# Kernel tuning notes

Hardware: AMD Instinct MI355X
Metric: run time of the kernel (lower is better)

Reference implementation:

```python
import jax, jax.numpy as jnp
import numpy as np

N = 1024
B = 128

def setup_inputs() -> dict:
    key = jax.random.key(0)
    k1, k2 = jax.random.split(key)
    log_alpha = jax.random.normal(k1, (B, N), dtype=jnp.float32)
    W = jax.random.normal(k2, (N, N), dtype=jnp.float32)  # unnormalized_transition_matrix
    return {"log_alpha": log_alpha, "W": W}

def reference(log_alpha, W):
    # log_softmax over dim=0 (columns) as in torch F.log_softmax(..., dim=0)
    log_T = jax.nn.log_softmax(W, axis=0)  # (N, N)
    # out[b, i] = logsumexp_k( log_T[i, k] + log_alpha[b, k] )
    # matches log_domain_matmul(log_T, log_alpha.T).T
    scores = log_T[None, :, :] + log_alpha[:, None, :]  # (B, N, N)
    out = jax.scipy.special.logsumexp(scores, axis=2)   # (B, N)
    return out
```

## Files before the change

### kernel.cpp

```cpp
#include <hip/hip_runtime.h>
#include <hip/hip_bf16.h>

#define N 1024
#define B 128

typedef __attribute__((ext_vector_type(8))) short short8;
typedef __attribute__((ext_vector_type(4))) float float4v;


__global__ void expw_colsum_kernel(const float* __restrict__ W,
                                   __hip_bfloat16* __restrict__ expW,
                                   float* __restrict__ pS) {
    int k  = blockIdx.x * 256 + threadIdx.x;
    int r0 = blockIdx.y * 16;
    float s = 0.f;
    #pragma unroll
    for (int r = r0; r < r0 + 16; ++r) {
        float e = __expf(W[r * N + k]);
        s += e;
        expW[r * N + k] = __float2bfloat16(e);
    }
    pS[blockIdx.y * N + k] = s;
}

__global__ void expa_kernel(const float* __restrict__ LA,
                            const float* __restrict__ pS,
                            __hip_bfloat16* __restrict__ expA) {
    int k = blockIdx.x * 256 + threadIdx.x;
    float S = 0.f;
    #pragma unroll
    for (int y = 0; y < 64; ++y) S += pS[y * N + k];
    float inv = __frcp_rn(S);
    int b0 = blockIdx.y * 4;
    #pragma unroll
    for (int b = b0; b < b0 + 4; ++b)
        expA[b * N + k] = __float2bfloat16(__expf(LA[b * N + k]) * inv);
}

__global__ void lse_gemm_kernel(const __hip_bfloat16* __restrict__ expA,
                                const __hip_bfloat16* __restrict__ expW,
                                float* __restrict__ out) {
    int lane = threadIdx.x & 63;
    int wave = threadIdx.x >> 6;
    int i0 = (blockIdx.x >> 1) * 16;
    int b0 = ((blockIdx.x & 1) * 4 + wave) * 16;
    int row  = lane & 15;
    int quad = lane >> 4;

    const short* aP = (const short*)(expA + (b0 + row) * N + quad * 8);
    const short* bP = (const short*)(expW + (i0 + row) * N + quad * 8);

    float4v acc = {0.f, 0.f, 0.f, 0.f};
    #pragma unroll 8
    for (int kk = 0; kk < N; kk += 32) {
        short8 af = *(const short8*)(aP + kk);
        short8 bf = *(const short8*)(bP + kk);
        acc = __builtin_amdgcn_mfma_f32_16x16x32_bf16(af, bf, acc, 0, 0, 0);
    }

    #pragma unroll
    for (int r = 0; r < 4; ++r) {
        int bb = b0 + quad * 4 + r;
        out[bb * N + i0 + row] = __logf(acc[r]);
    }
}

extern "C" void kernel_launch(void* const* d_in, const int* in_sizes, int n_in,
                              void* d_out, int out_size, void* d_ws, size_t ws_size,
                              hipStream_t stream) {
    const float* LA = (const float*)d_in[0];
    const float* W  = (const float*)d_in[1];
    float* out = (float*)d_out;

    char* ws = (char*)d_ws;
    float* pS = (float*)(ws);
    __hip_bfloat16* expW = (__hip_bfloat16*)(ws + 262144);
    __hip_bfloat16* expA = (__hip_bfloat16*)(ws + 262144 + 2097152);

    expw_colsum_kernel<<<dim3(4, 64), 256, 0, stream>>>(W, expW, pS);
    expa_kernel<<<dim3(4, 32), 256, 0, stream>>>(LA, pS, expA);
    lse_gemm_kernel<<<128, 256, 0, stream>>>(expA, expW, out);
}
```

Baseline: 83.86 us.

## Fuse three kernels into one persistent kernel with software grid barriers

Merges the exp/column-sum, alpha-normalization and bf16 MFMA GEMM kernels into a single 256-block launch separated by atomic sense-reversal grid barriers. The aim is to remove the cost of two extra kernel launches and the gaps between them. It depends on all 256 blocks being co-resident to avoid deadlock, and adds spin-wait and fence overhead while only 128 blocks do work in the GEMM phase.

```diff
diff --git a/kernel.cpp b/kernel.cpp
--- a/kernel.cpp
+++ b/kernel.cpp
@@ -8,60 +8,88 @@
 typedef __attribute__((ext_vector_type(4))) float float4v;
 
 
-__global__ void expw_colsum_kernel(const float* __restrict__ W,
-                                   __hip_bfloat16* __restrict__ expW,
-                                   float* __restrict__ pS) {
-    int k  = blockIdx.x * 256 + threadIdx.x;
-    int r0 = blockIdx.y * 16;
-    float s = 0.f;
-    #pragma unroll
-    for (int r = r0; r < r0 + 16; ++r) {
-        float e = __expf(W[r * N + k]);
-        s += e;
-        expW[r * N + k] = __float2bfloat16(e);
+__device__ __attribute__((aligned(128))) int g_arrive = 0;
+__device__ __attribute__((aligned(128))) int g_sense  = 0;
+
+__device__ __forceinline__ void grid_barrier() {
+    __syncthreads();
+    if (threadIdx.x == 0) {
+        __threadfence();
+        int epoch = __hip_atomic_load(&g_sense, __ATOMIC_RELAXED, __HIP_MEMORY_SCOPE_AGENT);
+        int prev  = __hip_atomic_fetch_add(&g_arrive, 1, __ATOMIC_ACQ_REL, __HIP_MEMORY_SCOPE_AGENT);
+        if (prev == (int)gridDim.x - 1) {
+            __hip_atomic_store(&g_arrive, 0, __ATOMIC_RELAXED, __HIP_MEMORY_SCOPE_AGENT);
+            __hip_atomic_store(&g_sense, epoch + 1, __ATOMIC_RELEASE, __HIP_MEMORY_SCOPE_AGENT);
+        } else {
+            while (__hip_atomic_load(&g_sense, __ATOMIC_ACQUIRE, __HIP_MEMORY_SCOPE_AGENT) == epoch)
+                __builtin_amdgcn_s_sleep(1);
+        }
+        __threadfence();
     }
-    pS[blockIdx.y * N + k] = s;
+    __syncthreads();
 }
 
-__global__ void expa_kernel(const float* __restrict__ LA,
-                            const float* __restrict__ pS,
-                            __hip_bfloat16* __restrict__ expA) {
-    int k = blockIdx.x * 256 + threadIdx.x;
-    float S = 0.f;
-    #pragma unroll
-    for (int y = 0; y < 64; ++y) S += pS[y * N + k];
-    float inv = __frcp_rn(S);
-    int b0 = blockIdx.y * 4;
-    #pragma unroll
-    for (int b = b0; b < b0 + 4; ++b)
-        expA[b * N + k] = __float2bfloat16(__expf(LA[b * N + k]) * inv);
-}
+__global__ void __launch_bounds__(256) fused_kernel(
+    const float* __restrict__ LA, const float* __restrict__ W,
+    float* __restrict__ out, float* __restrict__ pS,
+    __hip_bfloat16* __restrict__ expW, __hip_bfloat16* __restrict__ expA)
+{
+    const int tid = threadIdx.x;
+    const int blk = blockIdx.x;
 
-__global__ void lse_gemm_kernel(const __hip_bfloat16* __restrict__ expA,
-                                const __hip_bfloat16* __restrict__ expW,
-                                float* __restrict__ out) {
-    int lane = threadIdx.x & 63;
-    int wave = threadIdx.x >> 6;
-    int i0 = (blockIdx.x >> 1) * 16;
-    int b0 = ((blockIdx.x & 1) * 4 + wave) * 16;
-    int row  = lane & 15;
-    int quad = lane >> 4;
-
-    const short* aP = (const short*)(expA + (b0 + row) * N + quad * 8);
-    const short* bP = (const short*)(expW + (i0 + row) * N + quad * 8);
-
-    float4v acc = {0.f, 0.f, 0.f, 0.f};
-    #pragma unroll 8
-    for (int kk = 0; kk < N; kk += 32) {
-        short8 af = *(const short8*)(aP + kk);
-        short8 bf = *(const short8*)(bP + kk);
-        acc = __builtin_amdgcn_mfma_f32_16x16x32_bf16(af, bf, acc, 0, 0, 0);
+    {
+        int k  = (blk & 3) * 256 + tid;
+        int r0 = (blk >> 2) * 16;
+        float s = 0.f;
+        #pragma unroll
+        for (int r = r0; r < r0 + 16; ++r) {
+            float e = __expf(W[r * N + k]);
+            s += e;
+            expW[r * N + k] = __float2bfloat16(e);
+        }
+        pS[(blk >> 2) * N + k] = s;
     }
 
-    #pragma unroll
-    for (int r = 0; r < 4; ++r) {
-        int bb = b0 + quad * 4 + r;
-        out[bb * N + i0 + row] = __logf(acc[r]);
+    grid_barrier();
+
+    {
+        int k = (blk & 3) * 256 + tid;
+        float S = 0.f;
+        #pragma unroll
+        for (int y = 0; y < 64; ++y) S += pS[y * N + k];
+        float inv = __frcp_rn(S);
+        int b0 = (blk >> 2) * 2;
+        #pragma unroll
+        for (int b = b0; b < b0 + 2; ++b)
+            expA[b * N + k] = __float2bfloat16(__expf(LA[b * N + k]) * inv);
+    }
+
+    grid_barrier();
+
+    if (blk < 128) {
+        int lane = tid & 63;
+        int wave = tid >> 6;
+        int i0 = (blk >> 1) * 16;
+        int b0 = ((blk & 1) * 4 + wave) * 16;
+        int row  = lane & 15;
+        int quad = lane >> 4;
+
+        const short* aP = (const short*)(expA + (b0 + row) * N + quad * 8);
+        const short* bP = (const short*)(expW + (i0 + row) * N + quad * 8);
+
+        float4v acc = {0.f, 0.f, 0.f, 0.f};
+        #pragma unroll 8
+        for (int kk = 0; kk < N; kk += 32) {
+            short8 af = *(const short8*)(aP + kk);
+            short8 bf = *(const short8*)(bP + kk);
+            acc = __builtin_amdgcn_mfma_f32_16x16x32_bf16(af, bf, acc, 0, 0, 0);
+        }
+
+        #pragma unroll
+        for (int r = 0; r < 4; ++r) {
+            int bb = b0 + quad * 4 + r;
+            out[bb * N + i0 + row] = __logf(acc[r]);
+        }
     }
 }
 
@@ -77,7 +105,5 @@
     __hip_bfloat16* expW = (__hip_bfloat16*)(ws + 262144);
     __hip_bfloat16* expA = (__hip_bfloat16*)(ws + 262144 + 2097152);
 
-    expw_colsum_kernel<<<dim3(4, 64), 256, 0, stream>>>(W, expW, pS);
-    expa_kernel<<<dim3(4, 32), 256, 0, stream>>>(LA, pS, expA);
-    lse_gemm_kernel<<<128, 256, 0, stream>>>(expA, expW, out);
+    fused_kernel<<<256, 256, 0, stream>>>(LA, W, out, pS, expW, expA);
 }
```

Result: slower. 123.8 us (+47.6%).

## Fuse exp of W and log_alpha into GEMM kernel, drop intermediate bf16 buffers

Applied to the files above, without the earlier changes.

Removes the expA kernel and the bf16 expW write. The GEMM kernel now computes exp(W) for its 16 rows directly into XOR-swizzled shared memory, and the column-sum reciprocals into shared memory. It also computes exp(log_alpha)*invS on the fly for the A operand. This cuts one launch and the global round-trips of the intermediates, at the cost of redundant exp work: each W row tile is exponentiated by two blocks, and each block recomputes all 1024 inverse sums from 64 partials.

```diff
diff --git a/kernel.cpp b/kernel.cpp
--- a/kernel.cpp
+++ b/kernel.cpp
@@ -8,53 +8,78 @@
 typedef __attribute__((ext_vector_type(4))) float float4v;
 
 
-__global__ void expw_colsum_kernel(const float* __restrict__ W,
-                                   __hip_bfloat16* __restrict__ expW,
-                                   float* __restrict__ pS) {
+static __device__ __forceinline__ short bf16bits(float x) {
+    union { __hip_bfloat16 h; short s; } u;
+    u.h = __float2bfloat16(x);
+    return u.s;
+}
+
+__global__ void __launch_bounds__(256) colsum_kernel(const float* __restrict__ W,
+                                                     float* __restrict__ pS) {
     int k  = blockIdx.x * 256 + threadIdx.x;
     int r0 = blockIdx.y * 16;
     float s = 0.f;
     #pragma unroll
-    for (int r = r0; r < r0 + 16; ++r) {
-        float e = __expf(W[r * N + k]);
-        s += e;
-        expW[r * N + k] = __float2bfloat16(e);
-    }
+    for (int r = r0; r < r0 + 16; ++r)
+        s += __expf(W[r * N + k]);
     pS[blockIdx.y * N + k] = s;
 }
 
-__global__ void expa_kernel(const float* __restrict__ LA,
-                            const float* __restrict__ pS,
-                            __hip_bfloat16* __restrict__ expA) {
-    int k = blockIdx.x * 256 + threadIdx.x;
-    float S = 0.f;
+__global__ void __launch_bounds__(256) lse_kernel(const float* __restrict__ LA,
+                                                  const float* __restrict__ W,
+                                                  const float* __restrict__ pS,
+                                                  float* __restrict__ out) {
+    __shared__ float invS[N];
+    __shared__ short bt[16 * N];
+
+    const int tid = threadIdx.x;
+    const int i0  = (blockIdx.x >> 1) * 16;
+
     #pragma unroll
-    for (int y = 0; y < 64; ++y) S += pS[y * N + k];
-    float inv = __frcp_rn(S);
-    int b0 = blockIdx.y * 4;
-    #pragma unroll
-    for (int b = b0; b < b0 + 4; ++b)
-        expA[b * N + k] = __float2bfloat16(__expf(LA[b * N + k]) * inv);
-}
+    for (int r = 0; r < 16; ++r) {
+        #pragma unroll
+        for (int j = 0; j < 4; ++j) {
+            int c = j * 256 + tid;
+            float e = __expf(W[(i0 + r) * N + c]);
+            int byte = ((r * N + c) * 2) ^ ((r & 7) << 4);
+            *(short*)((char*)bt + byte) = bf16bits(e);
+        }
+    }
 
-__global__ void lse_gemm_kernel(const __hip_bfloat16* __restrict__ expA,
-                                const __hip_bfloat16* __restrict__ expW,
-                                float* __restrict__ out) {
-    int lane = threadIdx.x & 63;
-    int wave = threadIdx.x >> 6;
-    int i0 = (blockIdx.x >> 1) * 16;
-    int b0 = ((blockIdx.x & 1) * 4 + wave) * 16;
+    for (int k = tid; k < N; k += 256) {
+        float s = 0.f;
+        #pragma unroll
+        for (int y = 0; y < 64; ++y) s += pS[y * N + k];
+        invS[k] = __frcp_rn(s);
+    }
+    __syncthreads();
+
+    int lane = tid & 63;
+    int wave = tid >> 6;
+    int b0   = (blockIdx.x & 1) * 64 + wave * 16;
     int row  = lane & 15;
     int quad = lane >> 4;
+    const int xm = (row & 7) << 4;
 
-    const short* aP = (const short*)(expA + (b0 + row) * N + quad * 8);
-    const short* bP = (const short*)(expW + (i0 + row) * N + quad * 8);
+    const float* aP = LA + (b0 + row) * N + quad * 8;
+    const float* sP = invS + quad * 8;
+    const char*  bB = (const char*)bt;
 
     float4v acc = {0.f, 0.f, 0.f, 0.f};
     #pragma unroll 8
     for (int kk = 0; kk < N; kk += 32) {
-        short8 af = *(const short8*)(aP + kk);
-        short8 bf = *(const short8*)(bP + kk);
+        float4v a0 = *(const float4v*)(aP + kk);
+        float4v a1 = *(const float4v*)(aP + kk + 4);
+        float4v s0 = *(const float4v*)(sP + kk);
+        float4v s1 = *(const float4v*)(sP + kk + 4);
+        int bByte = ((row * N + quad * 8 + kk) * 2) ^ xm;
+        short8 bf = *(const short8*)(bB + bByte);
+        short8 af;
+        #pragma unroll
+        for (int j = 0; j < 4; ++j) {
+            af[j]     = bf16bits(__expf(a0[j]) * s0[j]);
+            af[j + 4] = bf16bits(__expf(a1[j]) * s1[j]);
+        }
         acc = __builtin_amdgcn_mfma_f32_16x16x32_bf16(af, bf, acc, 0, 0, 0);
     }
 
@@ -72,12 +97,8 @@
     const float* W  = (const float*)d_in[1];
     float* out = (float*)d_out;
 
-    char* ws = (char*)d_ws;
-    float* pS = (float*)(ws);
-    __hip_bfloat16* expW = (__hip_bfloat16*)(ws + 262144);
-    __hip_bfloat16* expA = (__hip_bfloat16*)(ws + 262144 + 2097152);
+    float* pS = (float*)d_ws;
 
-    expw_colsum_kernel<<<dim3(4, 64), 256, 0, stream>>>(W, expW, pS);
-    expa_kernel<<<dim3(4, 32), 256, 0, stream>>>(LA, pS, expA);
-    lse_gemm_kernel<<<128, 256, 0, stream>>>(expA, expW, out);
+    colsum_kernel<<<dim3(4, 64), 256, 0, stream>>>(W, pS);
+    lse_kernel<<<128, 256, 0, stream>>>(LA, W, pS, out);
 }
```

Result: faster. 82.18 us (-2.0%).
